# Kernel tuning notes

Measured on AMD Instinct MI355X. Metric: run time of the kernel, lower is better.

Reference implementation:

```python
import jax, jax.numpy as jnp
import numpy as np
from jax import lax


def setup_inputs() -> dict:
    key = jax.random.key(0)
    x = jax.random.normal(key, (8, 128, 256, 256), dtype=jnp.float32)
    return {"x": x}


def reference(x) -> jnp.ndarray:
    # Vertical line (corner-style) pool: running maximum along the vertical
    # (H) axis, scanning from bottom to top, i.e. out[..., i, :] = max_{j>=i} x[..., j, :].
    # Implemented as an associative scan with max, reversed along axis=2 (H of NCHW).
    return lax.associative_scan(jnp.maximum, x, axis=2, reverse=True)
```

## Files before the change

### kernel.cpp

```cpp
#include <hip/hip_runtime.h>
#include <hip/hip_bf16.h>
#include <math.h>


#define H 256
#define W 256

typedef float f32x4 __attribute__((ext_vector_type(4)));

__global__ __launch_bounds__(256) void VerticalLinePool_kernel(
    const float* __restrict__ x, float* __restrict__ out) {
    const int lane = threadIdx.x & 63;
    const int wv   = threadIdx.x >> 6;
    const int slab = blockIdx.x * 4 + wv;

    const size_t base = (size_t)slab * (H * W) + (size_t)lane * 4;
    const f32x4* __restrict__ xp = (const f32x4*)(x + base);
    f32x4* __restrict__ op = (f32x4*)(out + base);

    f32x4 acc = (f32x4)(-INFINITY);

#pragma unroll 16
    for (int h = H - 1; h >= 0; --h) {
        f32x4 v = __builtin_nontemporal_load(&xp[(size_t)h * (W / 4)]);
        acc.x = fmaxf(acc.x, v.x);
        acc.y = fmaxf(acc.y, v.y);
        acc.z = fmaxf(acc.z, v.z);
        acc.w = fmaxf(acc.w, v.w);
        __builtin_nontemporal_store(acc, &op[(size_t)h * (W / 4)]);
    }
}

extern "C" void kernel_launch(void* const* d_in, const int* in_sizes, int n_in,
                              void* d_out, int out_size, void* d_ws, size_t ws_size,
                              hipStream_t stream) {
    const float* x = (const float*)d_in[0];
    float* out = (float*)d_out;
    const int slabs = in_sizes[0] / (H * W);
    VerticalLinePool_kernel<<<slabs / 4, 256, 0, stream>>>(x, out);
}
```

Before: 432.4 us.

## Double-buffer row loads in register tiles to overlap loads with scan

Measured after the change: 439.1 us. Within noise of the previous version (+1.5%).

```diff
diff --git a/kernel.cpp b/kernel.cpp
--- a/kernel.cpp
+++ b/kernel.cpp
@@ -5,8 +5,19 @@
 
 #define H 256
 #define W 256
+#define T 16
+#define RS (W / 4)
 
 typedef float f32x4 __attribute__((ext_vector_type(4)));
+
+__device__ __forceinline__ f32x4 max4(f32x4 a, f32x4 b) {
+    f32x4 r;
+    r.x = fmaxf(a.x, b.x);
+    r.y = fmaxf(a.y, b.y);
+    r.z = fmaxf(a.z, b.z);
+    r.w = fmaxf(a.w, b.w);
+    return r;
+}
 
 __global__ __launch_bounds__(256) void VerticalLinePool_kernel(
     const float* __restrict__ x, float* __restrict__ out) {
@@ -18,17 +29,35 @@
     const f32x4* __restrict__ xp = (const f32x4*)(x + base);
     f32x4* __restrict__ op = (f32x4*)(out + base);
 
+    f32x4 A[T], B[T];
     f32x4 acc = (f32x4)(-INFINITY);
 
-#pragma unroll 16
-    for (int h = H - 1; h >= 0; --h) {
-        f32x4 v = __builtin_nontemporal_load(&xp[(size_t)h * (W / 4)]);
-        acc.x = fmaxf(acc.x, v.x);
-        acc.y = fmaxf(acc.y, v.y);
-        acc.z = fmaxf(acc.z, v.z);
-        acc.w = fmaxf(acc.w, v.w);
-        __builtin_nontemporal_store(acc, &op[(size_t)h * (W / 4)]);
+#define LOAD(buf, t)                                              \
+    _Pragma("unroll")                                             \
+    for (int i = 0; i < T; ++i)                                   \
+        buf[i] = xp[(size_t)((t) * T + i) * RS];
+
+#define CONSUME(buf, t)                                           \
+    _Pragma("unroll")                                             \
+    for (int i = T - 1; i >= 0; --i) {                            \
+        acc = max4(acc, buf[i]);                                  \
+        buf[i] = acc;                                             \
+    }                                                             \
+    _Pragma("unroll")                                             \
+    for (int i = 0; i < T; ++i)                                   \
+        op[(size_t)((t) * T + i) * RS] = buf[i];
+
+    LOAD(A, 15);
+#pragma unroll
+    for (int t = 15; t >= 1; t -= 2) {
+        LOAD(B, t - 1);
+        CONSUME(A, t);
+        if (t - 2 >= 0) { LOAD(A, t - 2); }
+        CONSUME(B, t - 1);
     }
+
+#undef LOAD
+#undef CONSUME
 }
 
 extern "C" void kernel_launch(void* const* d_in, const int* in_sizes, int n_in,
```

## Split vertical max-scan across 16 waves per slab with shared-memory carry

Applied to the files above, without the earlier changes.

Result: slower. 451.1 us (+4.3%).

```diff
diff --git a/kernel.cpp b/kernel.cpp
--- a/kernel.cpp
+++ b/kernel.cpp
@@ -5,29 +5,55 @@
 
 #define H 256
 #define W 256
+#define CH 16
+#define NW 16
+#define RS (W / 4)
 
 typedef float f32x4 __attribute__((ext_vector_type(4)));
 
-__global__ __launch_bounds__(256) void VerticalLinePool_kernel(
+__device__ __forceinline__ f32x4 max4(f32x4 a, f32x4 b) {
+    f32x4 r;
+    r.x = fmaxf(a.x, b.x);
+    r.y = fmaxf(a.y, b.y);
+    r.z = fmaxf(a.z, b.z);
+    r.w = fmaxf(a.w, b.w);
+    return r;
+}
+
+__global__ __launch_bounds__(1024, 8) void VerticalLinePool_kernel(
     const float* __restrict__ x, float* __restrict__ out) {
     const int lane = threadIdx.x & 63;
     const int wv   = threadIdx.x >> 6;
-    const int slab = blockIdx.x * 4 + wv;
+    const int slab = blockIdx.x;
 
-    const size_t base = (size_t)slab * (H * W) + (size_t)lane * 4;
+    const size_t base = (size_t)slab * (H * W) + (size_t)(wv * CH) * W + (size_t)lane * 4;
     const f32x4* __restrict__ xp = (const f32x4*)(x + base);
     f32x4* __restrict__ op = (f32x4*)(out + base);
 
-    f32x4 acc = (f32x4)(-INFINITY);
+    f32x4 s[CH];
+#pragma unroll
+    for (int i = 0; i < CH; ++i) {
+        s[i] = xp[(size_t)i * RS];
+    }
 
-#pragma unroll 16
-    for (int h = H - 1; h >= 0; --h) {
-        f32x4 v = __builtin_nontemporal_load(&xp[(size_t)h * (W / 4)]);
-        acc.x = fmaxf(acc.x, v.x);
-        acc.y = fmaxf(acc.y, v.y);
-        acc.z = fmaxf(acc.z, v.z);
-        acc.w = fmaxf(acc.w, v.w);
-        __builtin_nontemporal_store(acc, &op[(size_t)h * (W / 4)]);
+    f32x4 run = (f32x4)(-INFINITY);
+#pragma unroll
+    for (int i = CH - 1; i >= 0; --i) {
+        run = max4(run, s[i]);
+        s[i] = run;
+    }
+
+    __shared__ f32x4 tot[NW][64];
+    tot[wv][lane] = run;
+    __syncthreads();
+
+    f32x4 M = (f32x4)(-INFINITY);
+    for (int k = wv + 1; k < NW; ++k)
+        M = max4(M, tot[k][lane]);
+
+#pragma unroll
+    for (int i = 0; i < CH; ++i) {
+        op[(size_t)i * RS] = max4(s[i], M);
     }
 }
 
@@ -37,5 +63,5 @@
     const float* x = (const float*)d_in[0];
     float* out = (float*)d_out;
     const int slabs = in_sizes[0] / (H * W);
-    VerticalLinePool_kernel<<<slabs / 4, 256, 0, stream>>>(x, out);
+    VerticalLinePool_kernel<<<slabs, 1024, 0, stream>>>(x, out);
 }
```
